# Performance work log

Measured on AMD Instinct MI355X. Metric: run time of the kernel, lower is better.

Reference implementation:

```python
import jax, jax.numpy as jnp
import numpy as np

B, S, HID = 2, 1024, 2048
HQ, HKV, HD = 32, 8, 64
ROPE_BASE = 10000.0

def _rope_tables(seq_len, head_dim):
    inv_freq = 1.0 / (ROPE_BASE ** (np.arange(0, head_dim, 2, dtype=np.float32) / head_dim))
    t = np.arange(seq_len, dtype=np.float32)
    freqs = np.outer(t, inv_freq)                      # [S, d/2]
    emb = np.concatenate([freqs, freqs], axis=-1)      # [S, d]
    return jnp.asarray(np.cos(emb)), jnp.asarray(np.sin(emb))

def setup_inputs() -> dict:
    key = jax.random.key(0)
    ks = jax.random.split(key, 5)
    cos, sin = _rope_tables(S, HD)
    return {
        'hidden_states': jax.random.normal(ks[0], (B, S, HID), jnp.float32),
        'cos': cos, 'sin': sin,
        'Wq': jax.random.normal(ks[1], (HID, HID), jnp.float32) * (HID ** -0.5),
        'Wk': jax.random.normal(ks[2], (HID, HKV * HD), jnp.float32) * (HID ** -0.5),
        'Wv': jax.random.normal(ks[3], (HID, HKV * HD), jnp.float32) * (HID ** -0.5),
        'Wo': jax.random.normal(ks[4], (HID, HID), jnp.float32) * (HID ** -0.5),
    }

def _rotate_half(x):
    d = x.shape[-1]
    return jnp.concatenate([-x[..., d // 2:], x[..., :d // 2]], axis=-1)

def reference(hidden_states, cos, sin, Wq, Wk, Wv, Wo):
    b, s, _ = hidden_states.shape
    q = (hidden_states @ Wq).reshape(b, s, HQ, HD)    # [b,s,Hq,d]
    k = (hidden_states @ Wk).reshape(b, s, HKV, HD)   # [b,s,Hkv,d]
    v = (hidden_states @ Wv).reshape(b, s, HKV, HD)
    # RoPE: cos/sin [s,d] broadcast as [s,1,d] over head dim
    c = cos[:, None, :]
    sn = sin[:, None, :]
    q = q * c + _rotate_half(q) * sn
    k = k * c + _rotate_half(k) * sn
    # GQA: expand kv heads to query heads (repeat_kv)
    n_rep = HQ // HKV
    k = jnp.repeat(k, n_rep, axis=2)                  # [b,s,Hq,d]
    v = jnp.repeat(v, n_rep, axis=2)
    scale = HD ** -0.5
    scores = jnp.einsum('bqhd,bkhd->bhqk', q, k) * scale  # [b,Hq,s,s]
    causal = jnp.tril(jnp.ones((s, s), bool))
    scores = jnp.where(causal, scores, jnp.float32(-1e30))
    probs = jax.nn.softmax(scores.astype(jnp.float32), axis=-1).astype(q.dtype)
    out = jnp.einsum('bhqk,bkhd->bqhd', probs, v).reshape(b, s, HID)
    return out @ Wo
```

## Files before the change

### kernel.cpp

```cpp
#include <hip/hip_runtime.h>
#include <math.h>

#define B_   2
#define S_   1024
#define HID_ 2048
#define HQ_  32
#define HKV_ 8
#define HD_  64
#define NQKV 3072

#define PCHUNK 2097152

using short8  = __attribute__((ext_vector_type(8))) short;
using floatx4 = __attribute__((ext_vector_type(4))) float;

__device__ __forceinline__ unsigned short f2bf(float x) {
    unsigned int u = __builtin_bit_cast(unsigned int, x);
    u += 0x7FFFu + ((u >> 16) & 1u);
    return (unsigned short)(u >> 16);
}
__device__ __forceinline__ float bf2f(unsigned short u) {
    return __builtin_bit_cast(float, (unsigned int)u << 16);
}

__device__ __forceinline__ void gl_lds16(const unsigned short* g, unsigned short* l) {
    __builtin_amdgcn_global_load_lds(
        (const __attribute__((address_space(1))) void*)g,
        (__attribute__((address_space(3))) void*)l, 16, 0, 0);
}

__global__ __launch_bounds__(256) void gemm_qkv(const unsigned short* __restrict__ A,
                                                const unsigned short* __restrict__ Bt,
                                                unsigned short* __restrict__ Qp,
                                                unsigned short* __restrict__ KVp) {
    __shared__ __align__(16) unsigned short As[128 * 64];
    __shared__ __align__(16) unsigned short Bs[128 * 64];

    int bid = blockIdx.x;
    int m0, n0, z, Nw, nc0;
    unsigned short* C;
    if (bid < 512) {
        n0 = (bid & 15) * 128; m0 = ((bid >> 4) & 15) * 128; z = bid >> 8;
        C = Qp + (size_t)z * 2048 * 2048; Nw = 2048; nc0 = n0;
    } else {
        bid -= 512;
        n0 = 2048 + (bid & 7) * 128; m0 = ((bid >> 3) & 15) * 128; z = bid >> 7;
        C = KVp + (size_t)z * 2048 * 1024; Nw = 1024; nc0 = n0 - 2048;
    }
    const int kbase = z * 1024;

    const int tid  = threadIdx.x;
    const int w    = tid >> 6;
    const int lane = tid & 63;
    const int col  = lane & 15;
    const int quad = lane >> 4;
    const int wm = (w >> 1) * 64;
    const int wn = (w & 1) * 64;

    const int srow = lane >> 3;
    const int scol = ((lane & 7) ^ srow) * 8;
    const unsigned short* Ag = A  + (size_t)(m0 + w * 32 + srow) * HID_ + scol;
    const unsigned short* Bg = Bt + (size_t)(n0 + w * 32 + srow) * HID_ + scol;

    floatx4 acc[4][4] = {};

    for (int k0 = kbase; k0 < kbase + 1024; k0 += 64) {
#pragma unroll
        for (int c = 0; c < 4; ++c) {
            gl_lds16(Ag + (size_t)(8 * c) * HID_ + k0, &As[(w * 32 + 8 * c) * 64]);
            gl_lds16(Bg + (size_t)(8 * c) * HID_ + k0, &Bs[(w * 32 + 8 * c) * 64]);
        }
        __syncthreads();

#pragma unroll
        for (int hh = 0; hh < 2; ++hh) {
            short8 af[4], bfr[4];
#pragma unroll
            for (int i = 0; i < 4; ++i)
                af[i] = *(const short8*)&As[(wm + i * 16 + col) * 64
                                            + (((hh * 4 + quad) ^ (col & 7)) << 3)];
#pragma unroll
            for (int j = 0; j < 4; ++j)
                bfr[j] = *(const short8*)&Bs[(wn + j * 16 + col) * 64
                                             + (((hh * 4 + quad) ^ (col & 7)) << 3)];
#pragma unroll
            for (int i = 0; i < 4; ++i)
#pragma unroll
                for (int j = 0; j < 4; ++j)
                    acc[i][j] = __builtin_amdgcn_mfma_f32_16x16x32_bf16(
                        af[i], bfr[j], acc[i][j], 0, 0, 0);
        }
        __syncthreads();
    }

#pragma unroll
    for (int i = 0; i < 4; ++i)
#pragma unroll
        for (int j = 0; j < 4; ++j)
#pragma unroll
            for (int r = 0; r < 4; ++r)
                C[(size_t)(m0 + wm + i * 16 + quad * 4 + r) * Nw
                  + (nc0 + wn + j * 16 + col)] = f2bf(acc[i][j][r]);
}

__global__ __launch_bounds__(256) void gemm_wo(const unsigned short* __restrict__ A,
                                               const unsigned short* __restrict__ Bt,
                                               float* __restrict__ Cf,
                                               unsigned short* __restrict__ Cp1) {
    __shared__ __align__(16) unsigned short As[128 * 64];
    __shared__ __align__(16) unsigned short Bs[128 * 64];

    const int m0 = blockIdx.y * 128;
    const int n0 = blockIdx.x * 128;
    const int z  = blockIdx.z;
    const int kbase = z * 1024;

    const int tid  = threadIdx.x;
    const int w    = tid >> 6;
    const int lane = tid & 63;
    const int col  = lane & 15;
    const int quad = lane >> 4;
    const int wm = (w >> 1) * 64;
    const int wn = (w & 1) * 64;

    const int srow = lane >> 3;
    const int scol = ((lane & 7) ^ srow) * 8;
    const unsigned short* Ag = A  + (size_t)(m0 + w * 32 + srow) * HID_ + scol;
    const unsigned short* Bg = Bt + (size_t)(n0 + w * 32 + srow) * HID_ + scol;

    floatx4 acc[4][4] = {};

    for (int k0 = kbase; k0 < kbase + 1024; k0 += 64) {
#pragma unroll
        for (int c = 0; c < 4; ++c) {
            gl_lds16(Ag + (size_t)(8 * c) * HID_ + k0, &As[(w * 32 + 8 * c) * 64]);
            gl_lds16(Bg + (size_t)(8 * c) * HID_ + k0, &Bs[(w * 32 + 8 * c) * 64]);
        }
        __syncthreads();

#pragma unroll
        for (int hh = 0; hh < 2; ++hh) {
            short8 af[4], bfr[4];
#pragma unroll
            for (int i = 0; i < 4; ++i)
                af[i] = *(const short8*)&As[(wm + i * 16 + col) * 64
                                            + (((hh * 4 + quad) ^ (col & 7)) << 3)];
#pragma unroll
            for (int j = 0; j < 4; ++j)
                bfr[j] = *(const short8*)&Bs[(wn + j * 16 + col) * 64
                                             + (((hh * 4 + quad) ^ (col & 7)) << 3)];
#pragma unroll
            for (int i = 0; i < 4; ++i)
#pragma unroll
                for (int j = 0; j < 4; ++j)
                    acc[i][j] = __builtin_amdgcn_mfma_f32_16x16x32_bf16(
                        af[i], bfr[j], acc[i][j], 0, 0, 0);
        }
        __syncthreads();
    }

#pragma unroll
    for (int i = 0; i < 4; ++i)
#pragma unroll
        for (int j = 0; j < 4; ++j)
#pragma unroll
            for (int r = 0; r < 4; ++r) {
                size_t off = (size_t)(m0 + wm + i * 16 + quad * 4 + r) * HID_
                           + (n0 + wn + j * 16 + col);
                if (z == 0) Cf[off] = acc[i][j][r];
                else        Cp1[off] = f2bf(acc[i][j][r]);
            }
}

__global__ __launch_bounds__(256) void reduce_wo(float* __restrict__ out,
                                                 const unsigned short* __restrict__ p1) {
    int i4 = (blockIdx.x * 256 + threadIdx.x) * 4;
    float4 o = *(float4*)&out[i4];
    ushort4 p = *(const ushort4*)&p1[i4];
    o.x += bf2f(p.x); o.y += bf2f(p.y); o.z += bf2f(p.z); o.w += bf2f(p.w);
    *(float4*)&out[i4] = o;
}

__global__ __launch_bounds__(256) void prep(const float* __restrict__ X,
                                            const float* __restrict__ Wq,
                                            const float* __restrict__ Wk,
                                            const float* __restrict__ Wv,
                                            const float* __restrict__ Wo,
                                            unsigned short* __restrict__ Xbf,
                                            unsigned short* __restrict__ WcatT,
                                            unsigned short* __restrict__ WoT) {
    __shared__ float tile[32][33];
    int bid = blockIdx.x;
    if (bid < 4096) {
        int tid = bid * 256 + threadIdx.x;
        float4 v = *(const float4*)&X[(size_t)tid * 4];
        ushort4 o = {f2bf(v.x), f2bf(v.y), f2bf(v.z), f2bf(v.w)};
        *(ushort4*)&Xbf[(size_t)tid * 4] = o;
        return;
    }
    const float* W;
    unsigned short* WT;
    int N, tn0, tk0;
    if (bid < 10240) {
        bid -= 4096;
        if (bid < 4096) {
            W = Wq; WT = WcatT; N = HID_;
            tn0 = (bid & 63) * 32; tk0 = (bid >> 6) * 32;
        } else if (bid < 5120) {
            bid -= 4096;
            W = Wk; WT = WcatT + (size_t)HID_ * HID_; N = 512;
            tn0 = (bid & 15) * 32; tk0 = (bid >> 4) * 32;
        } else {
            bid -= 5120;
            W = Wv; WT = WcatT + (size_t)(HID_ + 512) * HID_; N = 512;
            tn0 = (bid & 15) * 32; tk0 = (bid >> 4) * 32;
        }
    } else {
        bid -= 10240;
        W = Wo; WT = WoT; N = HID_;
        tn0 = (bid & 63) * 32; tk0 = (bid >> 6) * 32;
    }
    const int r  = threadIdx.x >> 3;
    const int c4 = (threadIdx.x & 7) * 4;
    float4 v = *(const float4*)&W[(size_t)(tk0 + r) * N + tn0 + c4];
    tile[r][c4 + 0] = v.x;
    tile[r][c4 + 1] = v.y;
    tile[r][c4 + 2] = v.z;
    tile[r][c4 + 3] = v.w;
    __syncthreads();
    ushort4 o = {f2bf(tile[c4 + 0][r]), f2bf(tile[c4 + 1][r]),
                 f2bf(tile[c4 + 2][r]), f2bf(tile[c4 + 3][r])};
    *(ushort4*)&WT[(size_t)(tn0 + r) * HID_ + tk0 + c4] = o;
}

__global__ __launch_bounds__(256) void transpose_wo(const float* __restrict__ Wo,
                                                    unsigned short* __restrict__ WoT) {
    __shared__ float tile[32][33];
    int bid = blockIdx.x;
    const int tn0 = (bid & 63) * 32;
    const int tk0 = (bid >> 6) * 32;
    const int r  = threadIdx.x >> 3;
    const int c4 = (threadIdx.x & 7) * 4;
    float4 v = *(const float4*)&Wo[(size_t)(tk0 + r) * HID_ + tn0 + c4];
    tile[r][c4 + 0] = v.x;
    tile[r][c4 + 1] = v.y;
    tile[r][c4 + 2] = v.z;
    tile[r][c4 + 3] = v.w;
    __syncthreads();
    ushort4 o = {f2bf(tile[c4 + 0][r]), f2bf(tile[c4 + 1][r]),
                 f2bf(tile[c4 + 2][r]), f2bf(tile[c4 + 3][r])};
    *(ushort4*)&WoT[(size_t)(tn0 + r) * HID_ + tk0 + c4] = o;
}

__global__ __launch_bounds__(256) void convert_qkv(const unsigned short* __restrict__ Qp,
                                                   const unsigned short* __restrict__ KVp,
                                                   const float* __restrict__ cosT,
                                                   const float* __restrict__ sinT,
                                                   unsigned short* __restrict__ Qbf,
                                                   unsigned short* __restrict__ Kbf,
                                                   unsigned short* __restrict__ Vt) {
    const size_t QSTR  = (size_t)2048 * 2048;
    const size_t KVSTR = (size_t)2048 * 1024;
    int tid = blockIdx.x * 256 + threadIdx.x;
    const int NQ4 = 524288;
    const int NK4 = 131072;
    if (tid < NQ4) {
        int d0 = (tid & 7) * 4;
        int h  = (tid >> 3) & 31;
        int s  = (tid >> 8) & 1023;
        int b  = tid >> 18;
        const unsigned short* row = Qp + (size_t)(b * S_ + s) * 2048 + h * HD_;
        ushort4 a0 = *(const ushort4*)&row[d0];
        ushort4 a1 = *(const ushort4*)&row[d0 + 32];
        ushort4 p0 = *(const ushort4*)&row[QSTR + d0];
        ushort4 p1 = *(const ushort4*)&row[QSTR + d0 + 32];
        float4 c0  = *(const float4*)&cosT[s * HD_ + d0];
        float4 sn0 = *(const float4*)&sinT[s * HD_ + d0];
        float4 c1  = *(const float4*)&cosT[s * HD_ + d0 + 32];
        float4 sn1 = *(const float4*)&sinT[s * HD_ + d0 + 32];
        ushort4 o0, o1;
#pragma unroll
        for (int j = 0; j < 4; ++j) {
            float x0 = bf2f(((const unsigned short*)&a0)[j]) +
                       bf2f(((const unsigned short*)&p0)[j]);
            float x1 = bf2f(((const unsigned short*)&a1)[j]) +
                       bf2f(((const unsigned short*)&p1)[j]);
            ((unsigned short*)&o0)[j] =
                f2bf((x0 * ((const float*)&c0)[j] - x1 * ((const float*)&sn0)[j]) * 0.125f);
            ((unsigned short*)&o1)[j] =
                f2bf((x1 * ((const float*)&c1)[j] + x0 * ((const float*)&sn1)[j]) * 0.125f);
        }
        unsigned short* orow = Qbf + ((size_t)(b * HQ_ + h) * S_ + s) * HD_;
        *(ushort4*)&orow[d0]      = o0;
        *(ushort4*)&orow[d0 + 32] = o1;
    } else if (tid < NQ4 + NK4) {
        tid -= NQ4;
        int d0 = (tid & 7) * 4;
        int kv = (tid >> 3) & 7;
        int s  = (tid >> 6) & 1023;
        int b  = tid >> 16;
        const unsigned short* row = KVp + (size_t)(b * S_ + s) * 1024 + kv * HD_;
        ushort4 a0 = *(const ushort4*)&row[d0];
        ushort4 a1 = *(const ushort4*)&row[d0 + 32];
        ushort4 p0 = *(const ushort4*)&row[KVSTR + d0];
        ushort4 p1 = *(const ushort4*)&row[KVSTR + d0 + 32];
        float4 c0  = *(const float4*)&cosT[s * HD_ + d0];
        float4 sn0 = *(const float4*)&sinT[s * HD_ + d0];
        float4 c1  = *(const float4*)&cosT[s * HD_ + d0 + 32];
        float4 sn1 = *(const float4*)&sinT[s * HD_ + d0 + 32];
        ushort4 o0, o1;
#pragma unroll
        for (int j = 0; j < 4; ++j) {
            float x0 = bf2f(((const unsigned short*)&a0)[j]) +
                       bf2f(((const unsigned short*)&p0)[j]);
            float x1 = bf2f(((const unsigned short*)&a1)[j]) +
                       bf2f(((const unsigned short*)&p1)[j]);
            ((unsigned short*)&o0)[j] =
                f2bf(x0 * ((const float*)&c0)[j] - x1 * ((const float*)&sn0)[j]);
            ((unsigned short*)&o1)[j] =
                f2bf(x1 * ((const float*)&c1)[j] + x0 * ((const float*)&sn1)[j]);
        }
        unsigned short* orow = Kbf + ((size_t)(b * HKV_ + kv) * S_ + s) * HD_;
        *(ushort4*)&orow[d0]      = o0;
        *(ushort4*)&orow[d0 + 32] = o1;
    } else {
        tid -= NQ4 + NK4;
        int s4 = tid & 255;
        int d  = (tid >> 8) & (HD_ - 1);
        int kv = (tid >> 14) & (HKV_ - 1);
        int b  = tid >> 17;
        int s  = s4 * 4;
        const unsigned short* base =
            KVp + ((size_t)(b * S_ + s)) * 1024 + 512 + kv * HD_ + d;
        ushort4 o;
#pragma unroll
        for (int j = 0; j < 4; ++j) {
            float v = bf2f(base[(size_t)j * 1024]) +
                      bf2f(base[KVSTR + (size_t)j * 1024]);
            ((unsigned short*)&o)[j] = f2bf(v);
        }
        *(ushort4*)&Vt[((size_t)(b * HKV_ + kv) * HD_ + d) * S_ + s] = o;
    }
}

__global__ __launch_bounds__(256) void attn_mfma(const unsigned short* __restrict__ Qbf,
                                                 const unsigned short* __restrict__ Kbf,
                                                 const unsigned short* __restrict__ Vt,
                                                 unsigned short* __restrict__ Ctx,
                                                 float* __restrict__ PO,
                                                 float* __restrict__ ML) {
    const int x  = blockIdx.x;
    const int kv = blockIdx.y;
    const int b  = blockIdx.z;

    int tq, chunk, it0, it1;
    if (x < 32) {
        tq = 16 + (x >> 1); chunk = x & 1;
        const int ns = (32 * tq + 95) >> 6;
        const int hh = ns >> 1;
        it0 = chunk ? hh : 0;
        it1 = chunk ? ns : hh;
    } else {
        tq = 47 - x; chunk = -1;
        it0 = 0;
        it1 = (32 * tq + 95) >> 6;
    }

    const int w    = threadIdx.x >> 6;
    const int lane = threadIdx.x & 63;
    const int col  = lane & 15;
    const int quad = lane >> 4;

    const int h   = kv * 4 + w;
    const int bh  = b * HQ_ + h;
    const int bkv = b * HKV_ + kv;
    const int qw  = 32 * tq;

    __shared__ __align__(16) unsigned short sK[2][64 * 64];
    __shared__ __align__(16) unsigned short sV[2][64 * 64];
    __shared__ __align__(16) unsigned short sP[4][16 * 64];
    unsigned short* myP = sP[w];

    short8 bq[2][2];
#pragma unroll
    for (int u = 0; u < 2; ++u) {
        const unsigned short* qrow = Qbf + ((size_t)bh * S_ + qw + 16 * u + col) * HD_;
        bq[u][0] = *(const short8*)&qrow[quad * 8];
        bq[u][1] = *(const short8*)&qrow[32 + quad * 8];
    }

    const unsigned short* Kbase = Kbf + (size_t)bkv * S_ * HD_;
    const unsigned short* Vbase = Vt  + (size_t)bkv * HD_ * S_;

    const int sr  = lane >> 3;
    const int ssl = (lane & 7) ^ sr;
    const int r0  = 16 * w;

    floatx4 acc[2][4] = {};
    float m_i[2] = {-1e30f, -1e30f};
    float l_i[2] = {0.f, 0.f};

    {
        const int kb = it0 * 64;
#pragma unroll
        for (int c = 0; c < 2; ++c) {
            const int row = r0 + 8 * c + sr;
            gl_lds16(Kbase + (size_t)(kb + row) * HD_ + ssl * 8, &sK[0][(r0 + 8 * c) * 64]);
            gl_lds16(Vbase + (size_t)row * S_ + kb + ssl * 8,    &sV[0][(r0 + 8 * c) * 64]);
        }
    }
    __syncthreads();

    int cur = 0;
    for (int it = it0; it < it1; ++it) {
        const int k0 = it * 64;

        if (it + 1 < it1) {
            const int kn = k0 + 64;
#pragma unroll
            for (int c = 0; c < 2; ++c) {
                const int row = r0 + 8 * c + sr;
                gl_lds16(Kbase + (size_t)(kn + row) * HD_ + ssl * 8,
                         &sK[cur ^ 1][(r0 + 8 * c) * 64]);
                gl_lds16(Vbase + (size_t)row * S_ + kn + ssl * 8,
                         &sV[cur ^ 1][(r0 + 8 * c) * 64]);
            }
        }

        floatx4 sc[2][4];
        __builtin_amdgcn_s_setprio(1);
#pragma unroll
        for (int tt = 0; tt < 4; ++tt) {
            const int krow = 16 * tt + col;
            const unsigned short* kr = &sK[cur][krow * 64];
            short8 ak0 = *(const short8*)&kr[((quad    ) ^ (krow & 7)) * 8];
            short8 ak1 = *(const short8*)&kr[((quad + 4) ^ (krow & 7)) * 8];
#pragma unroll
            for (int u = 0; u < 2; ++u) {
                floatx4 z = {0.f, 0.f, 0.f, 0.f};
                z = __builtin_amdgcn_mfma_f32_16x16x32_bf16(ak0, bq[u][0], z, 0, 0, 0);
                z = __builtin_amdgcn_mfma_f32_16x16x32_bf16(ak1, bq[u][1], z, 0, 0, 0);
                sc[u][tt] = z;
            }
        }
        __builtin_amdgcn_s_setprio(0);

        short8 pa[2][2];
#pragma unroll
        for (int u = 0; u < 2; ++u) {
            const int qbase = qw + 16 * u;
            const int myq   = qbase + col;
            if (k0 + 63 > qbase) {
#pragma unroll
                for (int tt = 0; tt < 4; ++tt)
#pragma unroll
                    for (int r = 0; r < 4; ++r)
                        if (k0 + 16 * tt + quad * 4 + r > myq) sc[u][tt][r] = -1e30f;
            }
            float vmax = sc[u][0][0];
#pragma unroll
            for (int tt = 0; tt < 4; ++tt)
#pragma unroll
                for (int r = 0; r < 4; ++r)
                    vmax = fmaxf(vmax, sc[u][tt][r]);
            vmax = fmaxf(vmax, __shfl_xor(vmax, 16, 64));
            vmax = fmaxf(vmax, __shfl_xor(vmax, 32, 64));

            if (!__all(vmax <= m_i[u] + 8.0f)) {
                const float mnew  = fmaxf(m_i[u], vmax);
                const float alpha = __expf(m_i[u] - mnew);
                m_i[u] = mnew;
                l_i[u] *= alpha;
#pragma unroll
                for (int nt = 0; nt < 4; ++nt)
#pragma unroll
                    for (int r = 0; r < 4; ++r)
                        acc[u][nt][r] *= alpha;
            }
            const float mu = m_i[u];

            float lsum = 0.f;
#pragma unroll
            for (int tt = 0; tt < 4; ++tt) {
                float p0 = __expf(sc[u][tt][0] - mu);
                float p1 = __expf(sc[u][tt][1] - mu);
                float p2 = __expf(sc[u][tt][2] - mu);
                float p3 = __expf(sc[u][tt][3] - mu);
                lsum += (p0 + p1) + (p2 + p3);
                ushort4 pk = {f2bf(p0), f2bf(p1), f2bf(p2), f2bf(p3)};
                *(ushort4*)&myP[col * 64
                                + ((((4 * tt + quad) >> 1) ^ (col & 7)) << 3)
                                + (quad & 1) * 4] = pk;
            }
            lsum += __shfl_xor(lsum, 16, 64);
            lsum += __shfl_xor(lsum, 32, 64);
            l_i[u] += lsum;

            pa[u][0] = *(const short8*)&myP[col * 64 + (((quad    ) ^ (col & 7)) << 3)];
            pa[u][1] = *(const short8*)&myP[col * 64 + (((4 + quad) ^ (col & 7)) << 3)];
        }

        __builtin_amdgcn_s_setprio(1);
#pragma unroll
        for (int nt = 0; nt < 4; ++nt) {
            const int vrow = 16 * nt + col;
            const unsigned short* vr = &sV[cur][vrow * 64];
            short8 vb0 = *(const short8*)&vr[((quad    ) ^ (vrow & 7)) * 8];
            short8 vb1 = *(const short8*)&vr[((quad + 4) ^ (vrow & 7)) * 8];
#pragma unroll
            for (int u = 0; u < 2; ++u) {
                acc[u][nt] = __builtin_amdgcn_mfma_f32_16x16x32_bf16(vb0, pa[u][0], acc[u][nt], 0, 0, 0);
                acc[u][nt] = __builtin_amdgcn_mfma_f32_16x16x32_bf16(vb1, pa[u][1], acc[u][nt], 0, 0, 0);
            }
        }
        __builtin_amdgcn_s_setprio(0);

        __syncthreads();
        cur ^= 1;
    }

    if (chunk < 0) {
#pragma unroll
        for (int u = 0; u < 2; ++u) {
            const float invl = 1.0f / l_i[u];
            unsigned short* crow =
                Ctx + (size_t)(b * S_ + qw + 16 * u + col) * HID_ + h * HD_;
#pragma unroll
            for (int nt = 0; nt < 4; ++nt) {
                ushort4 o = {f2bf(acc[u][nt][0] * invl), f2bf(acc[u][nt][1] * invl),
                             f2bf(acc[u][nt][2] * invl), f2bf(acc[u][nt][3] * invl)};
                *(ushort4*)&crow[nt * 16 + quad * 4] = o;
            }
        }
    } else {
        const int ts = tq - 16;
        const int base_row = (((b * 8 + kv) * 16 + ts) * 4 + w) * 32;
        float* POc = PO + (size_t)chunk * PCHUNK;
#pragma unroll
        for (int u = 0; u < 2; ++u) {
            float* prow = &POc[(size_t)(base_row + 16 * u + col) * 64];
#pragma unroll
            for (int nt = 0; nt < 4; ++nt)
                *(floatx4*)&prow[nt * 16 + quad * 4] = acc[u][nt];
            if (quad == 0) {
                const int rr = chunk * 32768 + base_row + 16 * u + col;
                ML[rr * 2 + 0] = m_i[u];
                ML[rr * 2 + 1] = l_i[u];
            }
        }
    }
}

__global__ __launch_bounds__(256) void merge_attn(const float* __restrict__ PO,
                                                  const float* __restrict__ ML,
                                                  unsigned short* __restrict__ Ctx) {
    const int tid = blockIdx.x * 256 + threadIdx.x;
    const int i4  = tid * 4;
    const int row = i4 >> 6;
    const int d0  = i4 & 63;

    const float m0 = ML[row * 2 + 0];
    const float l0 = ML[row * 2 + 1];
    const float m1 = ML[(32768 + row) * 2 + 0];
    const float l1 = ML[(32768 + row) * 2 + 1];
    const float mf = fmaxf(m0, m1);
    const float s0 = __expf(m0 - mf);
    const float s1 = __expf(m1 - mf);
    const float inv = 1.0f / (l0 * s0 + l1 * s1);

    float4 o0 = *(const float4*)&PO[(size_t)row * 64 + d0];
    float4 o1 = *(const float4*)&PO[(size_t)PCHUNK + (size_t)row * 64 + d0];

    const int q  = row & 31;
    const int hh = (row >> 5) & 3;
    const int ts = (row >> 7) & 15;
    const int kv = (row >> 11) & 7;
    const int b  = row >> 14;
    const int q_abs = 512 + ts * 32 + q;
    const int h_abs = kv * 4 + hh;

    ushort4 o;
    o.x = f2bf((o0.x * s0 + o1.x * s1) * inv);
    o.y = f2bf((o0.y * s0 + o1.y * s1) * inv);
    o.z = f2bf((o0.z * s0 + o1.z * s1) * inv);
    o.w = f2bf((o0.w * s0 + o1.w * s1) * inv);
    *(ushort4*)&Ctx[((size_t)(b * S_ + q_abs)) * HID_ + h_abs * HD_ + d0] = o;
}

extern "C" void kernel_launch(void* const* d_in, const int* in_sizes, int n_in,
                              void* d_out, int out_size, void* d_ws, size_t ws_size,
                              hipStream_t stream) {
    const float* X    = (const float*)d_in[0];
    const float* cosT = (const float*)d_in[1];
    const float* sinT = (const float*)d_in[2];
    const float* Wq   = (const float*)d_in[3];
    const float* Wk   = (const float*)d_in[4];
    const float* Wv   = (const float*)d_in[5];
    const float* Wo   = (const float*)d_in[6];

    const int M = B_ * S_;
    const size_t MB = 1024u * 1024u;

    char* ws = (char*)d_ws;
    const bool bigws = ws_size >= 40 * MB;

    unsigned short* Xbf   = (unsigned short*)(ws);
    unsigned short* Qbf   = (unsigned short*)(ws);
    unsigned short* WcatT = (unsigned short*)(ws + 8 * MB);
    unsigned short* Kbf   = (unsigned short*)(ws + 8 * MB);
    unsigned short* Vt    = (unsigned short*)(ws + 10 * MB);
    unsigned short* WoT   = (unsigned short*)(ws + (bigws ? 28 : 12) * MB);
    float*          MLb   = (float*)(ws + (bigws ? 36 : 12) * MB);
    unsigned short* KVp   = (unsigned short*)(ws + 20 * MB);
    unsigned short* Ctxbf = (unsigned short*)(ws + 20 * MB);
    unsigned short* Wop1  = (unsigned short*)(ws);
    unsigned short* Qp    = (unsigned short*)d_out;
    float*          PO    = (float*)d_out;
    float* out = (float*)d_out;

    prep<<<bigws ? 14336 : 10240, 256, 0, stream>>>(X, Wq, Wk, Wv, Wo,
                                                    Xbf, WcatT, WoT);

    gemm_qkv<<<768, 256, 0, stream>>>(Xbf, WcatT, Qp, KVp);

    convert_qkv<<<3584, 256, 0, stream>>>(Qp, KVp, cosT, sinT, Qbf, Kbf, Vt);

    attn_mfma<<<dim3(48, HKV_, B_), 256, 0, stream>>>(Qbf, Kbf, Vt, Ctxbf,
                                                      PO, MLb);

    merge_attn<<<2048, 256, 0, stream>>>(PO, MLb, Ctxbf);

    if (!bigws)
        transpose_wo<<<4096, 256, 0, stream>>>(Wo, WoT);

    gemm_wo<<<dim3(16, 16, 2), 256, 0, stream>>>(Ctxbf, WoT, out, Wop1);

    reduce_wo<<<(M * HID_ / 4) / 256, 256, 0, stream>>>(out, Wop1);
}
```

Before: 229.2 us.

## Remap GEMM block order for XCD locality, use exp2 softmax, relayout workspace

Block indices of both GEMMs are permuted so consecutive blocks land on the same XCD (stride-8 interleave), aiming for better L2 reuse of shared A/B tiles. The query scale folds in log2(e) so softmax and merge use exp2f instead of __expf, saving a multiply per exponential. The workspace threshold and offsets are reorganised (bigws now needs 64MB, WoT and ML moved) with launch code split into two branches. If the workspace is between 40 and 64MB, the path now falls back to the on-the-fly Wo transpose.

After: 229.2 us. No clear change (+0.0%).

```diff
diff --git a/kernel.cpp b/kernel.cpp
--- a/kernel.cpp
+++ b/kernel.cpp
@@ -10,6 +10,7 @@
 #define NQKV 3072
 
 #define PCHUNK 2097152
+#define QSC   (0.125f * 1.44269504089f)
 
 using short8  = __attribute__((ext_vector_type(8))) short;
 using floatx4 = __attribute__((ext_vector_type(4))) float;
@@ -36,7 +37,7 @@
     __shared__ __align__(16) unsigned short As[128 * 64];
     __shared__ __align__(16) unsigned short Bs[128 * 64];
 
-    int bid = blockIdx.x;
+    int bid = (blockIdx.x & 7) * 96 + (blockIdx.x >> 3);
     int m0, n0, z, Nw, nc0;
     unsigned short* C;
     if (bid < 512) {
@@ -110,9 +111,10 @@
     __shared__ __align__(16) unsigned short As[128 * 64];
     __shared__ __align__(16) unsigned short Bs[128 * 64];
 
-    const int m0 = blockIdx.y * 128;
-    const int n0 = blockIdx.x * 128;
-    const int z  = blockIdx.z;
+    int bid = (blockIdx.x & 7) * 64 + (blockIdx.x >> 3);
+    const int z  = bid >> 8;
+    const int m0 = ((bid >> 4) & 15) * 128;
+    const int n0 = (bid & 15) * 128;
     const int kbase = z * 1024;
 
     const int tid  = threadIdx.x;
@@ -286,9 +288,9 @@
             float x1 = bf2f(((const unsigned short*)&a1)[j]) +
                        bf2f(((const unsigned short*)&p1)[j]);
             ((unsigned short*)&o0)[j] =
-                f2bf((x0 * ((const float*)&c0)[j] - x1 * ((const float*)&sn0)[j]) * 0.125f);
+                f2bf((x0 * ((const float*)&c0)[j] - x1 * ((const float*)&sn0)[j]) * QSC);
             ((unsigned short*)&o1)[j] =
-                f2bf((x1 * ((const float*)&c1)[j] + x0 * ((const float*)&sn1)[j]) * 0.125f);
+                f2bf((x1 * ((const float*)&c1)[j] + x0 * ((const float*)&sn1)[j]) * QSC);
         }
         unsigned short* orow = Qbf + ((size_t)(b * HQ_ + h) * S_ + s) * HD_;
         *(ushort4*)&orow[d0]      = o0;
@@ -468,7 +470,7 @@
 
             if (!__all(vmax <= m_i[u] + 8.0f)) {
                 const float mnew  = fmaxf(m_i[u], vmax);
-                const float alpha = __expf(m_i[u] - mnew);
+                const float alpha = exp2f(m_i[u] - mnew);
                 m_i[u] = mnew;
                 l_i[u] *= alpha;
 #pragma unroll
@@ -482,10 +484,10 @@
             float lsum = 0.f;
 #pragma unroll
             for (int tt = 0; tt < 4; ++tt) {
-                float p0 = __expf(sc[u][tt][0] - mu);
-                float p1 = __expf(sc[u][tt][1] - mu);
-                float p2 = __expf(sc[u][tt][2] - mu);
-                float p3 = __expf(sc[u][tt][3] - mu);
+                float p0 = exp2f(sc[u][tt][0] - mu);
+                float p1 = exp2f(sc[u][tt][1] - mu);
+                float p2 = exp2f(sc[u][tt][2] - mu);
+                float p3 = exp2f(sc[u][tt][3] - mu);
                 lsum += (p0 + p1) + (p2 + p3);
                 ushort4 pk = {f2bf(p0), f2bf(p1), f2bf(p2), f2bf(p3)};
                 *(ushort4*)&myP[col * 64
@@ -564,8 +566,8 @@
     const float m1 = ML[(32768 + row) * 2 + 0];
     const float l1 = ML[(32768 + row) * 2 + 1];
     const float mf = fmaxf(m0, m1);
-    const float s0 = __expf(m0 - mf);
-    const float s1 = __expf(m1 - mf);
+    const float s0 = exp2f(m0 - mf);
+    const float s1 = exp2f(m1 - mf);
     const float inv = 1.0f / (l0 * s0 + l1 * s1);
 
     float4 o0 = *(const float4*)&PO[(size_t)row * 64 + d0];
@@ -602,38 +604,54 @@
     const size_t MB = 1024u * 1024u;
 
     char* ws = (char*)d_ws;
-    const bool bigws = ws_size >= 40 * MB;
-
-    unsigned short* Xbf   = (unsigned short*)(ws);
-    unsigned short* Qbf   = (unsigned short*)(ws);
-    unsigned short* WcatT = (unsigned short*)(ws + 8 * MB);
-    unsigned short* Kbf   = (unsigned short*)(ws + 8 * MB);
-    unsigned short* Vt    = (unsigned short*)(ws + 10 * MB);
-    unsigned short* WoT   = (unsigned short*)(ws + (bigws ? 28 : 12) * MB);
-    float*          MLb   = (float*)(ws + (bigws ? 36 : 12) * MB);
-    unsigned short* KVp   = (unsigned short*)(ws + 20 * MB);
-    unsigned short* Ctxbf = (unsigned short*)(ws + 20 * MB);
-    unsigned short* Wop1  = (unsigned short*)(ws);
-    unsigned short* Qp    = (unsigned short*)d_out;
-    float*          PO    = (float*)d_out;
-    float* out = (float*)d_out;
-
-    prep<<<bigws ? 14336 : 10240, 256, 0, stream>>>(X, Wq, Wk, Wv, Wo,
-                                                    Xbf, WcatT, WoT);
-
-    gemm_qkv<<<768, 256, 0, stream>>>(Xbf, WcatT, Qp, KVp);
-
-    convert_qkv<<<3584, 256, 0, stream>>>(Qp, KVp, cosT, sinT, Qbf, Kbf, Vt);
-
-    attn_mfma<<<dim3(48, HKV_, B_), 256, 0, stream>>>(Qbf, Kbf, Vt, Ctxbf,
-                                                      PO, MLb);
-
-    merge_attn<<<2048, 256, 0, stream>>>(PO, MLb, Ctxbf);
-
-    if (!bigws)
+    const bool bigws = ws_size >= 64 * MB;
+
+    if (bigws) {
+        unsigned short* Xbf   = (unsigned short*)(ws);
+        unsigned short* Qbf   = (unsigned short*)(ws);
+        unsigned short* WcatT = (unsigned short*)(ws + 8 * MB);
+        unsigned short* Kbf   = (unsigned short*)(ws + 8 * MB);
+        unsigned short* Vt    = (unsigned short*)(ws + 10 * MB);
+        unsigned short* KVp   = (unsigned short*)(ws + 20 * MB);
+        unsigned short* Ctxbf = (unsigned short*)(ws + 20 * MB);
+        float*          MLb   = (float*)(ws + 45 * MB);
+        unsigned short* WoT   = (unsigned short*)(ws + 48 * MB);
+        unsigned short* Wop1  = (unsigned short*)(ws);
+        unsigned short* Qp    = (unsigned short*)d_out;
+        float*          PO    = (float*)d_out;
+        float* out = (float*)d_out;
+
+        prep<<<14336, 256, 0, stream>>>(X, Wq, Wk, Wv, Wo, Xbf, WcatT, WoT);
+        gemm_qkv<<<768, 256, 0, stream>>>(Xbf, WcatT, Qp, KVp);
+        convert_qkv<<<3584, 256, 0, stream>>>(Qp, KVp, cosT, sinT, Qbf, Kbf, Vt);
+        attn_mfma<<<dim3(48, HKV_, B_), 256, 0, stream>>>(Qbf, Kbf, Vt,
+                                                          Ctxbf, PO, MLb);
+        merge_attn<<<2048, 256, 0, stream>>>(PO, MLb, Ctxbf);
+        gemm_wo<<<512, 256, 0, stream>>>(Ctxbf, WoT, out, Wop1);
+        reduce_wo<<<(M * HID_ / 4) / 256, 256, 0, stream>>>(out, Wop1);
+    } else {
+        unsigned short* Xbf   = (unsigned short*)(ws);
+        unsigned short* Qbf   = (unsigned short*)(ws);
+        unsigned short* WcatT = (unsigned short*)(ws + 8 * MB);
+        unsigned short* Kbf   = (unsigned short*)(ws + 8 * MB);
+        unsigned short* Vt    = (unsigned short*)(ws + 10 * MB);
+        unsigned short* WoT   = (unsigned short*)(ws + 12 * MB);
+        float*          MLb   = (float*)(ws + 12 * MB);
+        unsigned short* KVp   = (unsigned short*)(ws + 20 * MB);
+        unsigned short* Ctxbf = (unsigned short*)(ws + 20 * MB);
+        unsigned short* Wop1  = (unsigned short*)(ws);
+        unsigned short* Qp    = (unsigned short*)d_out;
+        float*          PO    = (float*)d_out;
+        float* out = (float*)d_out;
+
+        prep<<<10240, 256, 0, stream>>>(X, Wq, Wk, Wv, Wo, Xbf, WcatT, WoT);
+        gemm_qkv<<<768, 256, 0, stream>>>(Xbf, WcatT, Qp, KVp);
+        convert_qkv<<<3584, 256, 0, stream>>>(Qp, KVp, cosT, sinT, Qbf, Kbf, Vt);
+        attn_mfma<<<dim3(48, HKV_, B_), 256, 0, stream>>>(Qbf, Kbf, Vt,
+                                                          Ctxbf, PO, MLb);
+        merge_attn<<<2048, 256, 0, stream>>>(PO, MLb, Ctxbf);
         transpose_wo<<<4096, 256, 0, stream>>>(Wo, WoT);
-
-    gemm_wo<<<dim3(16, 16, 2), 256, 0, stream>>>(Ctxbf, WoT, out, Wop1);
-
-    reduce_wo<<<(M * HID_ / 4) / 256, 256, 0, stream>>>(out, Wop1);
-}
+        gemm_wo<<<512, 256, 0, stream>>>(Ctxbf, WoT, out, Wop1);
+        reduce_wo<<<(M * HID_ / 4) / 256, 256, 0, stream>>>(out, Wop1);
+    }
+}
```
